# Kernel tuning notes

Measured on AMD Instinct MI355X. Metric: run time of the kernel, lower is better.

Reference implementation:

```python
import jax, jax.numpy as jnp
import numpy as np

B, D, F = 16384, 512, 28
GIN = D + D + F + 1  # 1053
EPS = 1e-5


def setup_inputs() -> dict:
    key = jax.random.key(0)
    ks = jax.random.split(key, 16)
    s = 0.02
    return {
        "team_embedding": jax.random.normal(ks[0], (B, D), jnp.float32),
        "opponent_embedding": jax.random.normal(ks[1], (B, D), jnp.float32),
        "game_features": jax.random.normal(ks[2], (B, F), jnp.float32),
        "won": jnp.round(jax.random.uniform(ks[3], (B, 1), jnp.float32)),
        # input_projection Linear(GIN -> D)
        "W_proj": jax.random.normal(ks[4], (D, GIN), jnp.float32) * s,
        "b_proj": jnp.zeros((D,), jnp.float32),
        # GRUCell params (PyTorch layout: [3D, *] with r,z,n blocks)
        "W_ih": jax.random.normal(ks[5], (3 * D, D), jnp.float32) * s,
        "b_ih": jnp.zeros((3 * D,), jnp.float32),
        "W_hh": jax.random.normal(ks[6], (3 * D, D), jnp.float32) * s,
        "b_hh": jnp.zeros((3 * D,), jnp.float32),
        # LayerNorm
        "gamma": jnp.ones((D,), jnp.float32),
        "beta": jnp.zeros((D,), jnp.float32),
        # game_importance MLP: D -> 128 -> 1
        "W_imp1": jax.random.normal(ks[7], (128, D), jnp.float32) * s,
        "b_imp1": jnp.zeros((128,), jnp.float32),
        "W_imp2": jax.random.normal(ks[8], (1, 128), jnp.float32) * s,
        "b_imp2": jnp.zeros((1,), jnp.float32),
    }


def reference(team_embedding, opponent_embedding, game_features, won,
              W_proj, b_proj, W_ih, b_ih, W_hh, b_hh,
              gamma, beta, W_imp1, b_imp1, W_imp2, b_imp2):
    # combined: [B, 2D+F+1]
    x = jnp.concatenate([team_embedding, opponent_embedding, game_features, won], axis=-1)
    # input_projection: Linear -> ReLU (Dropout is identity in eval)
    projected = jax.nn.relu(x @ W_proj.T + b_proj)  # [B, D]
    # game_importance: Linear -> ReLU -> Linear -> Sigmoid
    importance = jax.nn.sigmoid(jax.nn.relu(projected @ W_imp1.T + b_imp1) @ W_imp2.T + b_imp2)  # [B, 1]
    # GRUCell (PyTorch math)
    gi = projected @ W_ih.T + b_ih          # [B, 3D]
    gh = team_embedding @ W_hh.T + b_hh     # [B, 3D]
    i_r, i_z, i_n = jnp.split(gi, 3, axis=-1)
    h_r, h_z, h_n = jnp.split(gh, 3, axis=-1)
    r = jax.nn.sigmoid(i_r + h_r)
    z = jax.nn.sigmoid(i_z + h_z)
    n = jnp.tanh(i_n + r * h_n)
    new_embedding = (1.0 - z) * n + z * team_embedding
    # gated blend
    updated = team_embedding + importance * (new_embedding - team_embedding)
    # LayerNorm
    mu = jnp.mean(updated, axis=-1, keepdims=True)
    var = jnp.mean(jnp.square(updated - mu), axis=-1, keepdims=True)
    updated = gamma * (updated - mu) * jax.lax.rsqrt(var + EPS) + beta
    game_context = jax.lax.stop_gradient(projected)  # .detach().clone()
    return (updated, game_context)
```

## Files before the change

### kernel.cpp

```cpp
#include <hip/hip_runtime.h>
#include <hip/hip_bf16.h>


#define NB 16384
#define GINP 1088

typedef __bf16 bf16x8 __attribute__((ext_vector_type(8)));
typedef float f32x4 __attribute__((ext_vector_type(4)));
typedef unsigned short ushort8 __attribute__((ext_vector_type(8)));

__device__ __forceinline__ void gload_lds16(const void* g, void* l) {
  __builtin_amdgcn_global_load_lds(
      (const __attribute__((address_space(1))) void*)g,
      (__attribute__((address_space(3))) void*)l, 16, 0, 0);
}
__device__ __forceinline__ bf16x8 ds_read128(const unsigned short* l) {
  f32x4 r;
  asm volatile("ds_read_b128 %0, %1"
               : "=v"(r)
               : "v"((const __attribute__((address_space(3))) void*)l));
  bf16x8 out;
  __builtin_memcpy(&out, &r, 16);
  return out;
}
__device__ __forceinline__ float sigmoidf_(float x) { return 1.0f / (1.0f + expf(-x)); }
__device__ __forceinline__ float bf2f(unsigned short u) {
  unsigned int x = ((unsigned int)u) << 16;
  float f; __builtin_memcpy(&f, &x, 4); return f;
}

__global__ __launch_bounds__(256) void prep_x2(
    const float* __restrict__ team, const float* __restrict__ opp,
    const float* __restrict__ gf, const float* __restrict__ won,
    __hip_bfloat16* __restrict__ X) {
  long idx = (long)blockIdx.x * 256 + threadIdx.x;
  if (idx >= (long)NB * 136) return;
  const int r = (int)(idx / 136);
  const int c8 = (int)(idx % 136) * 8;
  float v[8];
  if (c8 < 512) {
    float4 a = *(const float4*)&team[(size_t)r * 512 + c8];
    float4 b = *(const float4*)&team[(size_t)r * 512 + c8 + 4];
    v[0]=a.x; v[1]=a.y; v[2]=a.z; v[3]=a.w; v[4]=b.x; v[5]=b.y; v[6]=b.z; v[7]=b.w;
  } else if (c8 < 1024) {
    float4 a = *(const float4*)&opp[(size_t)r * 512 + (c8 - 512)];
    float4 b = *(const float4*)&opp[(size_t)r * 512 + (c8 - 512) + 4];
    v[0]=a.x; v[1]=a.y; v[2]=a.z; v[3]=a.w; v[4]=b.x; v[5]=b.y; v[6]=b.z; v[7]=b.w;
  } else if (c8 < 1048) {
    const int g0 = c8 - 1024;
#pragma unroll
    for (int e = 0; e < 8; ++e) v[e] = gf[(size_t)r * 28 + g0 + e];
  } else if (c8 == 1048) {
    v[0] = gf[(size_t)r * 28 + 24]; v[1] = gf[(size_t)r * 28 + 25];
    v[2] = gf[(size_t)r * 28 + 26]; v[3] = gf[(size_t)r * 28 + 27];
    v[4] = won[r]; v[5] = 0.f; v[6] = 0.f; v[7] = 0.f;
  } else {
#pragma unroll
    for (int e = 0; e < 8; ++e) v[e] = 0.f;
  }
  __hip_bfloat16 h[8];
#pragma unroll
  for (int e = 0; e < 8; ++e) h[e] = __float2bfloat16(v[e]);
  *(uint4*)&X[(size_t)r * GINP + c8] = *(const uint4*)h;
}

__global__ __launch_bounds__(256) void prep_w2(
    const float* __restrict__ Wproj, const float* __restrict__ Wih,
    const float* __restrict__ Whh, const float* __restrict__ Wimp1,
    const float* __restrict__ bih, const float* __restrict__ bhh,
    __hip_bfloat16* __restrict__ Wpb, __hip_bfloat16* __restrict__ Wrz,
    __hip_bfloat16* __restrict__ Wn, __hip_bfloat16* __restrict__ Wimp1b,
    float* __restrict__ bcat) {
  long idx = (long)blockIdx.x * 256 + threadIdx.x;
  if (idx < 512L * 1088) {
    int r = (int)(idx / 1088), c = (int)(idx % 1088);
    Wpb[idx] = __float2bfloat16(c < 1053 ? Wproj[(size_t)r * 1053 + c] : 0.f);
    return;
  }
  idx -= 512L * 1088;
  if (idx < 1024L * 1024) {
    int q = (int)(idx >> 10), c = (int)(idx & 1023);
    float v = (c < 512) ? Wih[(size_t)q * 512 + c] : Whh[(size_t)q * 512 + (c - 512)];
    Wrz[idx] = __float2bfloat16(v);
    return;
  }
  idx -= 1024L * 1024;
  if (idx < 1024L * 512) {
    int q = (int)(idx / 512), c = (int)(idx % 512);
    float v = (q < 512) ? Wih[(size_t)(1024 + q) * 512 + c]
                        : Whh[(size_t)(1024 + q - 512) * 512 + c];
    Wn[idx] = __float2bfloat16(v);
    return;
  }
  idx -= 1024L * 512;
  if (idx < 128L * 512) { Wimp1b[idx] = __float2bfloat16(Wimp1[idx]); return; }
  idx -= 128L * 512;
  if (idx < 2048) {
    int j = (int)idx;
    float v;
    if (j < 1024) v = bih[j] + bhh[j];
    else if (j < 1536) v = bih[j];
    else v = bhh[j - 512];
    bcat[j] = v;
  }
}

template <int MODE>
__global__ __launch_bounds__(512, 1) void gemm_dp3(
    const __hip_bfloat16* __restrict__ A0, int lda0,
    const __hip_bfloat16* __restrict__ A1, int lda1,
    const __hip_bfloat16* __restrict__ W0, const __hip_bfloat16* __restrict__ W1,
    const float* __restrict__ bias,
    float* __restrict__ Cf, __hip_bfloat16* __restrict__ Cb,
    int tilesN, int NTP) {
  __shared__ __align__(16) unsigned short ldsA[3 * 256 * 64];
  __shared__ __align__(16) unsigned short ldsB[3 * 128 * 64];

  const int tid = threadIdx.x;
  const int wid = tid >> 6, lane = tid & 63;
  const int wr = wid >> 1, wc = wid & 1;
  const int fl = lane & 15, kh = lane >> 4;

  int bid = blockIdx.x;
  { const int cpx = gridDim.x >> 3; bid = (bid & 7) * cpx + (bid >> 3); }
  const int tm = bid / tilesN, tn = bid % tilesN;
  const int m0 = tm * 256;

  const __hip_bfloat16* Wp; int ldw, NT;
  if (MODE == 0) { Wp = W0 + (size_t)tn * 128 * GINP; ldw = GINP; NT = NTP; }
  else {
    if (tn < 8) { Wp = W0 + (size_t)tn * 128 * 1024; ldw = 1024; NT = 16; }
    else        { Wp = W1 + (size_t)(tn - 8) * 128 * 512; ldw = 512; NT = 8; }
  }
  const float* bp = bias + tn * 128;

  const int prow_b = tid >> 3;
  const int gp = tid & 7;

  auto stageAB = [&](int s, int buf) {
    const int kW = s * 64;
    const __hip_bfloat16* Ap; int lda; int kA;
    if (MODE == 0) { Ap = A0; lda = lda0; kA = s * 64; }
    else if (tn < 8) {
      if (s < 8) { Ap = A0; lda = lda0; kA = s * 64; }
      else       { Ap = A1; lda = lda1; kA = (s - 8) * 64; }
    } else if (tn < 12) { Ap = A0; lda = lda0; kA = s * 64; }
    else                { Ap = A1; lda = lda1; kA = s * 64; }
    unsigned short* la = &ldsA[buf * (256 * 64)];
    unsigned short* lb = &ldsB[buf * (128 * 64)];
#pragma unroll
    for (int i = 0; i < 4; ++i) {
      const int prow = i * 64 + prow_b;
      const int gl = gp ^ (prow & 7);
      gload_lds16(Ap + (size_t)(m0 + prow) * lda + kA + gl * 8,
                  la + i * 4096 + wid * 512);
    }
#pragma unroll
    for (int i = 0; i < 2; ++i) {
      const int prow = i * 64 + prow_b;
      const int gl = gp ^ (prow & 7);
      gload_lds16(Wp + (size_t)prow * ldw + kW + gl * 8,
                  lb + i * 4096 + wid * 512);
    }
  };

  f32x4 acc[4][4];
#pragma unroll
  for (int m = 0; m < 4; ++m)
#pragma unroll
    for (int n = 0; n < 4; ++n) acc[m][n] = (f32x4){0.f, 0.f, 0.f, 0.f};

  stageAB(0, 0);
  stageAB(1, 1);

  for (int t = 0; t < NT; ++t) {
    const int cur = t % 3;
    if (t + 1 < NT) {
      asm volatile("s_waitcnt vmcnt(6)" ::: "memory");
    } else {
      asm volatile("s_waitcnt vmcnt(0)" ::: "memory");
    }
    __builtin_amdgcn_s_barrier();
    if (t + 2 < NT) stageAB(t + 2, (t + 2) % 3);

    const unsigned short* At = &ldsA[cur * (256 * 64)];
    const unsigned short* Bt = &ldsB[cur * (128 * 64)];
    bf16x8 af[2][4], bfr[2][4];
#pragma unroll
    for (int kk = 0; kk < 2; ++kk) {
#pragma unroll
      for (int m = 0; m < 4; ++m) {
        const int r = wr * 64 + m * 16 + fl;
        const int g = (kk * 4 + kh) ^ (r & 7);
        af[kk][m] = ds_read128(&At[r * 64 + g * 8]);
      }
#pragma unroll
      for (int n = 0; n < 4; ++n) {
        const int r = wc * 64 + n * 16 + fl;
        const int g = (kk * 4 + kh) ^ (r & 7);
        bfr[kk][n] = ds_read128(&Bt[r * 64 + g * 8]);
      }
    }
    asm volatile("s_waitcnt lgkmcnt(0)" ::: "memory");
    __builtin_amdgcn_sched_barrier(0);
    __builtin_amdgcn_s_setprio(1);
#pragma unroll
    for (int kk = 0; kk < 2; ++kk)
#pragma unroll
      for (int m = 0; m < 4; ++m)
#pragma unroll
        for (int n = 0; n < 4; ++n)
          acc[m][n] = __builtin_amdgcn_mfma_f32_16x16x32_bf16(af[kk][m], bfr[kk][n], acc[m][n], 0, 0, 0);
    __builtin_amdgcn_s_setprio(0);
  }

#pragma unroll
  for (int m = 0; m < 4; ++m)
#pragma unroll
    for (int n = 0; n < 4; ++n)
#pragma unroll
      for (int j = 0; j < 4; ++j) {
        const int lrow = wr * 64 + m * 16 + kh * 4 + j;
        const int lcol = wc * 64 + n * 16 + fl;
        const size_t grow = (size_t)(m0 + lrow);
        float v = acc[m][n][j] + bp[lcol];
        if (MODE == 0) {
          v = fmaxf(v, 0.f);
          Cf[grow * 512 + tn * 128 + lcol] = v;
          Cb[grow * 512 + tn * 128 + lcol] = __float2bfloat16(v);
        } else {
          Cb[grow * 2048 + tn * 128 + lcol] = __float2bfloat16(v);
        }
      }
}

__global__ __launch_bounds__(256, 2) void gemm_imp2(
    const __hip_bfloat16* __restrict__ A, const __hip_bfloat16* __restrict__ W,
    const float* __restrict__ bias, const float* __restrict__ w2,
    const float* __restrict__ b2, float* __restrict__ imp) {
  __shared__ __align__(16) unsigned short ldsA[64 * 64];
  __shared__ __align__(16) unsigned short ldsB[128 * 64];
  __shared__ float sdot[64];
  const int tid = threadIdx.x;
  const int w = tid >> 6, lane = tid & 63;
  const int wr = w >> 1, wc = w & 1;
  const int fl = lane & 15, kh = lane >> 4;
  const int srow = lane >> 3, scol = (lane & 7) * 8;
  const int m0 = blockIdx.x * 64;

  if (tid < 64) sdot[tid] = 0.f;

  f32x4 acc[2][4];
#pragma unroll
  for (int m = 0; m < 2; ++m)
#pragma unroll
    for (int n = 0; n < 4; ++n) acc[m][n] = (f32x4){0.f, 0.f, 0.f, 0.f};

  for (int kt = 0; kt < 8; ++kt) {
    const int k0 = kt * 64;
#pragma unroll
    for (int c = 0; c < 2; ++c) {
      const int rgrp = c * 4 + w;
      const int row = rgrp * 8 + srow;
      gload_lds16(A + (size_t)(m0 + row) * 512 + k0 + scol, (char*)ldsA + rgrp * 1024);
    }
#pragma unroll
    for (int c = 0; c < 4; ++c) {
      const int rgrp = c * 4 + w;
      const int row = rgrp * 8 + srow;
      gload_lds16(W + (size_t)row * 512 + k0 + scol, (char*)ldsB + rgrp * 1024);
    }
    __syncthreads();
#pragma unroll
    for (int kk = 0; kk < 2; ++kk) {
      bf16x8 af[2], bfr[4];
#pragma unroll
      for (int m = 0; m < 2; ++m)
        af[m] = *(const bf16x8*)&ldsA[(wr * 32 + m * 16 + fl) * 64 + kk * 32 + kh * 8];
#pragma unroll
      for (int n = 0; n < 4; ++n)
        bfr[n] = *(const bf16x8*)&ldsB[(wc * 64 + n * 16 + fl) * 64 + kk * 32 + kh * 8];
#pragma unroll
      for (int m = 0; m < 2; ++m)
#pragma unroll
        for (int n = 0; n < 4; ++n)
          acc[m][n] = __builtin_amdgcn_mfma_f32_16x16x32_bf16(af[m], bfr[n], acc[m][n], 0, 0, 0);
    }
    __syncthreads();
  }
#pragma unroll
  for (int m = 0; m < 2; ++m)
#pragma unroll
    for (int j = 0; j < 4; ++j) {
      float p = 0.f;
#pragma unroll
      for (int n = 0; n < 4; ++n) {
        const int lcol = wc * 64 + n * 16 + fl;
        const float v = fmaxf(acc[m][n][j] + bias[lcol], 0.f);
        p += v * w2[lcol];
      }
      atomicAdd(&sdot[wr * 32 + m * 16 + kh * 4 + j], p);
    }
  __syncthreads();
  if (tid < 64) imp[m0 + tid] = sigmoidf_(sdot[tid] + b2[0]);
}

__global__ __launch_bounds__(256) void fuse_final2(
    const float* __restrict__ team, const __hip_bfloat16* __restrict__ gg,
    const float* __restrict__ imp, const float* __restrict__ gamma,
    const float* __restrict__ beta, float* __restrict__ out) {
  const int row = blockIdx.x * 4 + (threadIdx.x >> 6);
  const int lane = threadIdx.x & 63;
  const size_t gb = (size_t)row * 2048 + lane * 8;
  ushort8 sr = *(const ushort8*)&gg[gb];
  ushort8 szv = *(const ushort8*)&gg[gb + 512];
  ushort8 inn = *(const ushort8*)&gg[gb + 1024];
  ushort8 hnn = *(const ushort8*)&gg[gb + 1536];
  float4 t0 = *(const float4*)&team[(size_t)row * 512 + lane * 8];
  float4 t1 = *(const float4*)&team[(size_t)row * 512 + lane * 8 + 4];
  const float im = imp[row];
  float tv[8] = {t0.x, t0.y, t0.z, t0.w, t1.x, t1.y, t1.z, t1.w};
  float u[8];
  float s = 0.f, ss = 0.f;
#pragma unroll
  for (int e = 0; e < 8; ++e) {
    const float rg = sigmoidf_(bf2f(sr[e]));
    const float zg = sigmoidf_(bf2f(szv[e]));
    const float ng = tanhf(bf2f(inn[e]) + rg * bf2f(hnn[e]));
    const float ne = (1.f - zg) * ng + zg * tv[e];
    const float uu = tv[e] + im * (ne - tv[e]);
    u[e] = uu; s += uu; ss += uu * uu;
  }
#pragma unroll
  for (int off = 32; off; off >>= 1) {
    s += __shfl_down(s, off);
    ss += __shfl_down(ss, off);
  }
  s = __shfl(s, 0); ss = __shfl(ss, 0);
  const float mu = s * (1.f / 512.f);
  const float inv = rsqrtf(ss * (1.f / 512.f) - mu * mu + 1e-5f);
  float4 g0 = *(const float4*)&gamma[lane * 8], g1 = *(const float4*)&gamma[lane * 8 + 4];
  float4 b0 = *(const float4*)&beta[lane * 8], b1 = *(const float4*)&beta[lane * 8 + 4];
  float gv[8] = {g0.x, g0.y, g0.z, g0.w, g1.x, g1.y, g1.z, g1.w};
  float bv[8] = {b0.x, b0.y, b0.z, b0.w, b1.x, b1.y, b1.z, b1.w};
  float4 o0, o1;
  o0.x = gv[0] * (u[0] - mu) * inv + bv[0];
  o0.y = gv[1] * (u[1] - mu) * inv + bv[1];
  o0.z = gv[2] * (u[2] - mu) * inv + bv[2];
  o0.w = gv[3] * (u[3] - mu) * inv + bv[3];
  o1.x = gv[4] * (u[4] - mu) * inv + bv[4];
  o1.y = gv[5] * (u[5] - mu) * inv + bv[5];
  o1.z = gv[6] * (u[6] - mu) * inv + bv[6];
  o1.w = gv[7] * (u[7] - mu) * inv + bv[7];
  *(float4*)&out[(size_t)row * 512 + lane * 8] = o0;
  *(float4*)&out[(size_t)row * 512 + lane * 8 + 4] = o1;
}

extern "C" void kernel_launch(void* const* d_in, const int* in_sizes, int n_in,
                              void* d_out, int out_size, void* d_ws, size_t ws_size,
                              hipStream_t stream) {
  const float* team   = (const float*)d_in[0];
  const float* opp    = (const float*)d_in[1];
  const float* gf     = (const float*)d_in[2];
  const float* won    = (const float*)d_in[3];
  const float* W_proj = (const float*)d_in[4];
  const float* b_proj = (const float*)d_in[5];
  const float* W_ih   = (const float*)d_in[6];
  const float* b_ih   = (const float*)d_in[7];
  const float* W_hh   = (const float*)d_in[8];
  const float* b_hh   = (const float*)d_in[9];
  const float* gamma  = (const float*)d_in[10];
  const float* beta   = (const float*)d_in[11];
  const float* W_imp1 = (const float*)d_in[12];
  const float* b_imp1 = (const float*)d_in[13];
  const float* W_imp2 = (const float*)d_in[14];
  const float* b_imp2 = (const float*)d_in[15];

  char* ws = (char*)d_ws;
  size_t o = 0;
  __hip_bfloat16* Xbf    = (__hip_bfloat16*)(ws + o); o += (size_t)NB * GINP * 2;
  __hip_bfloat16* Wpb    = (__hip_bfloat16*)(ws + o); o += (size_t)512 * GINP * 2;
  __hip_bfloat16* Wrz    = (__hip_bfloat16*)(ws + o); o += (size_t)1024 * 1024 * 2;
  __hip_bfloat16* Wn     = (__hip_bfloat16*)(ws + o); o += (size_t)1024 * 512 * 2;
  __hip_bfloat16* Wimp1b = (__hip_bfloat16*)(ws + o); o += (size_t)128 * 512 * 2;
  float*          bcat   = (float*)(ws + o);          o += (size_t)2048 * 4;
  __hip_bfloat16* Pbf    = (__hip_bfloat16*)(ws + o); o += (size_t)NB * 512 * 2;
  float*          imp    = (float*)(ws + o);          o += (size_t)NB * 4;
  __hip_bfloat16* gg     = (__hip_bfloat16*)(ws + o); o += (size_t)NB * 2048 * 2;

  float* out_updated = (float*)d_out;
  float* out_ctx     = (float*)d_out + (size_t)NB * 512;

  prep_x2<<<(NB * 136 + 255) / 256, 256, 0, stream>>>(team, opp, gf, won, Xbf);
  {
    const long total = 512L * 1088 + 1024L * 1024 + 1024L * 512 + 128L * 512 + 2048;
    prep_w2<<<(int)((total + 255) / 256), 256, 0, stream>>>(
        W_proj, W_ih, W_hh, W_imp1, b_ih, b_hh, Wpb, Wrz, Wn, Wimp1b, bcat);
  }
  gemm_dp3<0><<<256, 512, 0, stream>>>(Xbf, GINP, nullptr, 0, Wpb, nullptr, b_proj,
                                       out_ctx, Pbf, 4, 17);
  gemm_imp2<<<NB / 64, 256, 0, stream>>>(Pbf, Wimp1b, b_imp1, W_imp2, b_imp2, imp);
  gemm_dp3<2><<<1024, 512, 0, stream>>>(Pbf, 512, Xbf, GINP, Wrz, Wn, bcat,
                                        nullptr, gg, 16, 0);
  fuse_final2<<<NB / 4, 256, 0, stream>>>(team, gg, imp, gamma, beta, out_updated);
}
```

Before: 157.5 us.

## Replace GRU gate GEMM with 256x256-tile kernel using phased double-buffer schedule

Adds a dedicated GRU gate GEMM kernel with 256x256 output tiles (8 waves, each owning 128x64) instead of 256x128. It double-buffers LDS and splits each K-step into four MFMA phases, interleaving LDS reads and global prefetches between them. The goal is more arithmetic per byte loaded and better overlap of loads with MFMA. The larger tile raises register pressure (128 accumulator floats per lane) and halves the grid to 512 blocks, which may leave CUs unevenly loaded.

```diff
diff --git a/kernel.cpp b/kernel.cpp
--- a/kernel.cpp
+++ b/kernel.cpp
@@ -105,6 +105,158 @@
   }
 }
 
+__global__ __launch_bounds__(512, 1) void gemm_g8(
+    const __hip_bfloat16* __restrict__ Pm, const __hip_bfloat16* __restrict__ Xb,
+    const __hip_bfloat16* __restrict__ Wrz, const __hip_bfloat16* __restrict__ Wn,
+    const float* __restrict__ bcat, __hip_bfloat16* __restrict__ gg) {
+  __shared__ __align__(16) unsigned short ldsA[2 * 256 * 64];
+  __shared__ __align__(16) unsigned short ldsB[2 * 256 * 64];
+
+  const int tid = threadIdx.x;
+  const int wid = tid >> 6, lane = tid & 63;
+  const int wr = wid >> 2, wc = wid & 3;
+  const int fl = lane & 15, kh = lane >> 4;
+  const int srow = tid >> 3;
+  const int sgp = tid & 7;
+
+  const int tn = blockIdx.x & 7, tm = blockIdx.x >> 3;
+  const int m0 = tm * 256;
+
+  const __hip_bfloat16* Wp;
+  int ldw, NT;
+  if (tn < 4) { Wp = Wrz + (size_t)tn * 256 * 1024; ldw = 1024; NT = 16; }
+  else        { Wp = Wn + (size_t)(tn - 4) * 256 * 512; ldw = 512; NT = 8; }
+  const float* bp = bcat + tn * 256;
+
+  auto stageA64 = [&](int s, int r0) {
+    const __hip_bfloat16* Ap; int lda; int k0;
+    if (tn < 4) {
+      if (s < 8) { Ap = Pm; lda = 512; k0 = s * 64; }
+      else       { Ap = Xb; lda = GINP; k0 = (s - 8) * 64; }
+    } else if (tn < 6) { Ap = Pm; lda = 512; k0 = s * 64; }
+    else               { Ap = Xb; lda = GINP; k0 = s * 64; }
+    const int row = r0 + srow;
+    const int gl = sgp ^ (row & 7);
+    gload_lds16(Ap + (size_t)(m0 + row) * lda + k0 + gl * 8,
+                &ldsA[(s & 1) * 16384 + (r0 + (wid << 3)) * 64]);
+  };
+  auto stageB64 = [&](int s, int r0) {
+    const int row = r0 + srow;
+    const int gl = sgp ^ (row & 7);
+    gload_lds16(Wp + (size_t)row * ldw + s * 64 + gl * 8,
+                &ldsB[(s & 1) * 16384 + (r0 + (wid << 3)) * 64]);
+  };
+  auto readA = [&](int sl, int m, int kk) -> bf16x8 {
+    const int row = wr * 128 + m * 16 + fl;
+    const int g = (kk * 4 + kh) ^ (row & 7);
+    return ds_read128(&ldsA[sl + row * 64 + g * 8]);
+  };
+  auto readB = [&](int sl, int n, int kk) -> bf16x8 {
+    const int row = wc * 64 + n * 16 + fl;
+    const int g = (kk * 4 + kh) ^ (row & 7);
+    return ds_read128(&ldsB[sl + row * 64 + g * 8]);
+  };
+
+  f32x4 acc[8][4];
+#pragma unroll
+  for (int m = 0; m < 8; ++m)
+#pragma unroll
+    for (int n = 0; n < 4; ++n) acc[m][n] = (f32x4){0.f, 0.f, 0.f, 0.f};
+
+  stageA64(0, 0); stageA64(0, 64); stageA64(0, 128); stageA64(0, 192);
+  stageB64(0, 0); stageB64(0, 64); stageB64(0, 128); stageB64(0, 192);
+  stageA64(1, 0); stageA64(1, 64); stageA64(1, 128); stageA64(1, 192);
+  stageB64(1, 0); stageB64(1, 64); stageB64(1, 128); stageB64(1, 192);
+  asm volatile("s_waitcnt vmcnt(8)" ::: "memory");
+  __builtin_amdgcn_s_barrier();
+
+  for (int t = 0; t < NT; ++t) {
+    const int sl = (t & 1) * 16384;
+    const bool pf = (t + 2 < NT);
+    bf16x8 fa0[4][2], fa1[4][2], fb0[2][2], fb1[2][2];
+
+#pragma unroll
+    for (int m = 0; m < 4; ++m) { fa0[m][0] = readA(sl, m, 0); fa0[m][1] = readA(sl, m, 1); }
+#pragma unroll
+    for (int n = 0; n < 2; ++n) { fb0[n][0] = readB(sl, n, 0); fb0[n][1] = readB(sl, n, 1); }
+    __builtin_amdgcn_s_barrier();
+    asm volatile("s_waitcnt lgkmcnt(0)" ::: "memory");
+    __builtin_amdgcn_sched_barrier(0);
+    __builtin_amdgcn_s_setprio(1);
+#pragma unroll
+    for (int kk = 0; kk < 2; ++kk)
+#pragma unroll
+      for (int m = 0; m < 4; ++m)
+#pragma unroll
+        for (int n = 0; n < 2; ++n)
+          acc[m][n] = __builtin_amdgcn_mfma_f32_16x16x32_bf16(fa0[m][kk], fb0[n][kk], acc[m][n], 0, 0, 0);
+    __builtin_amdgcn_s_setprio(0);
+    __builtin_amdgcn_s_barrier();
+
+#pragma unroll
+    for (int m = 0; m < 4; ++m) { fa1[m][0] = readA(sl, m + 4, 0); fa1[m][1] = readA(sl, m + 4, 1); }
+    if (pf) { stageA64(t + 2, 0); stageA64(t + 2, 128); }
+    __builtin_amdgcn_s_barrier();
+    asm volatile("s_waitcnt lgkmcnt(0)" ::: "memory");
+    __builtin_amdgcn_sched_barrier(0);
+    __builtin_amdgcn_s_setprio(1);
+#pragma unroll
+    for (int kk = 0; kk < 2; ++kk)
+#pragma unroll
+      for (int m = 0; m < 4; ++m)
+#pragma unroll
+        for (int n = 0; n < 2; ++n)
+          acc[m + 4][n] = __builtin_amdgcn_mfma_f32_16x16x32_bf16(fa1[m][kk], fb0[n][kk], acc[m + 4][n], 0, 0, 0);
+    __builtin_amdgcn_s_setprio(0);
+    __builtin_amdgcn_s_barrier();
+
+#pragma unroll
+    for (int n = 0; n < 2; ++n) { fb1[n][0] = readB(sl, n + 2, 0); fb1[n][1] = readB(sl, n + 2, 1); }
+    if (pf) { stageA64(t + 2, 64); stageA64(t + 2, 192); }
+    __builtin_amdgcn_s_barrier();
+    asm volatile("s_waitcnt lgkmcnt(0)" ::: "memory");
+    __builtin_amdgcn_sched_barrier(0);
+    __builtin_amdgcn_s_setprio(1);
+#pragma unroll
+    for (int kk = 0; kk < 2; ++kk)
+#pragma unroll
+      for (int m = 0; m < 4; ++m)
+#pragma unroll
+        for (int n = 0; n < 2; ++n)
+          acc[m + 4][n + 2] = __builtin_amdgcn_mfma_f32_16x16x32_bf16(fa1[m][kk], fb1[n][kk], acc[m + 4][n + 2], 0, 0, 0);
+    __builtin_amdgcn_s_setprio(0);
+    __builtin_amdgcn_s_barrier();
+
+    if (pf) { stageB64(t + 2, 0); stageB64(t + 2, 64); stageB64(t + 2, 128); stageB64(t + 2, 192); }
+    __builtin_amdgcn_sched_barrier(0);
+    __builtin_amdgcn_s_barrier();
+    __builtin_amdgcn_s_setprio(1);
+#pragma unroll
+    for (int kk = 0; kk < 2; ++kk)
+#pragma unroll
+      for (int m = 0; m < 4; ++m)
+#pragma unroll
+        for (int n = 0; n < 2; ++n)
+          acc[m][n + 2] = __builtin_amdgcn_mfma_f32_16x16x32_bf16(fa0[m][kk], fb1[n][kk], acc[m][n + 2], 0, 0, 0);
+    __builtin_amdgcn_s_setprio(0);
+    if (pf) { asm volatile("s_waitcnt vmcnt(8)" ::: "memory"); }
+    else    { asm volatile("s_waitcnt vmcnt(0)" ::: "memory"); }
+    __builtin_amdgcn_s_barrier();
+  }
+
+#pragma unroll
+  for (int m = 0; m < 8; ++m)
+#pragma unroll
+    for (int n = 0; n < 4; ++n)
+#pragma unroll
+      for (int j = 0; j < 4; ++j) {
+        const int lrow = wr * 128 + m * 16 + kh * 4 + j;
+        const int lcol = wc * 64 + n * 16 + fl;
+        gg[(size_t)(m0 + lrow) * 2048 + tn * 256 + lcol] =
+            __float2bfloat16(acc[m][n][j] + bp[lcol]);
+      }
+}
+
 template <int MODE>
 __global__ __launch_bounds__(512, 1) void gemm_dp3(
     const __hip_bfloat16* __restrict__ A0, int lda0,
@@ -127,11 +279,7 @@
   const int m0 = tm * 256;
 
   const __hip_bfloat16* Wp; int ldw, NT;
-  if (MODE == 0) { Wp = W0 + (size_t)tn * 128 * GINP; ldw = GINP; NT = NTP; }
-  else {
-    if (tn < 8) { Wp = W0 + (size_t)tn * 128 * 1024; ldw = 1024; NT = 16; }
-    else        { Wp = W1 + (size_t)(tn - 8) * 128 * 512; ldw = 512; NT = 8; }
-  }
+  Wp = W0 + (size_t)tn * 128 * GINP; ldw = GINP; NT = NTP;
   const float* bp = bias + tn * 128;
 
   const int prow_b = tid >> 3;
@@ -139,13 +287,7 @@
 
   auto stageAB = [&](int s, int buf) {
     const int kW = s * 64;
-    const __hip_bfloat16* Ap; int lda; int kA;
-    if (MODE == 0) { Ap = A0; lda = lda0; kA = s * 64; }
-    else if (tn < 8) {
-      if (s < 8) { Ap = A0; lda = lda0; kA = s * 64; }
-      else       { Ap = A1; lda = lda1; kA = (s - 8) * 64; }
-    } else if (tn < 12) { Ap = A0; lda = lda0; kA = s * 64; }
-    else                { Ap = A1; lda = lda1; kA = s * 64; }
+    const __hip_bfloat16* Ap = A0; int lda = lda0; int kA = s * 64;
     unsigned short* la = &ldsA[buf * (256 * 64)];
     unsigned short* lb = &ldsB[buf * (128 * 64)];
 #pragma unroll
@@ -175,11 +317,8 @@
 
   for (int t = 0; t < NT; ++t) {
     const int cur = t % 3;
-    if (t + 1 < NT) {
-      asm volatile("s_waitcnt vmcnt(6)" ::: "memory");
-    } else {
-      asm volatile("s_waitcnt vmcnt(0)" ::: "memory");
-    }
+    if (t + 1 < NT) { asm volatile("s_waitcnt vmcnt(6)" ::: "memory"); }
+    else            { asm volatile("s_waitcnt vmcnt(0)" ::: "memory"); }
     __builtin_amdgcn_s_barrier();
     if (t + 2 < NT) stageAB(t + 2, (t + 2) % 3);
 
@@ -224,13 +363,9 @@
         const int lcol = wc * 64 + n * 16 + fl;
         const size_t grow = (size_t)(m0 + lrow);
         float v = acc[m][n][j] + bp[lcol];
-        if (MODE == 0) {
-          v = fmaxf(v, 0.f);
-          Cf[grow * 512 + tn * 128 + lcol] = v;
-          Cb[grow * 512 + tn * 128 + lcol] = __float2bfloat16(v);
-        } else {
-          Cb[grow * 2048 + tn * 128 + lcol] = __float2bfloat16(v);
-        }
+        v = fmaxf(v, 0.f);
+        Cf[grow * 512 + tn * 128 + lcol] = v;
+        Cb[grow * 512 + tn * 128 + lcol] = __float2bfloat16(v);
       }
 }
 
@@ -400,7 +535,6 @@
   gemm_dp3<0><<<256, 512, 0, stream>>>(Xbf, GINP, nullptr, 0, Wpb, nullptr, b_proj,
                                        out_ctx, Pbf, 4, 17);
   gemm_imp2<<<NB / 64, 256, 0, stream>>>(Pbf, Wimp1b, b_imp1, W_imp2, b_imp2, imp);
-  gemm_dp3<2><<<1024, 512, 0, stream>>>(Pbf, 512, Xbf, GINP, Wrz, Wn, bcat,
-                                        nullptr, gg, 16, 0);
+  gemm_g8<<<512, 512, 0, stream>>>(Pbf, Xbf, Wrz, Wn, bcat, gg);
   fuse_final2<<<NB / 4, 256, 0, stream>>>(team, gg, imp, gamma, beta, out_updated);
 }
```

Result: slower. 169.8 us (+7.8%).

## Shrink GEMM tiles to 128x128 with double buffering and merge prep kernels

Applied to the files above, without the earlier changes.

The GEMM kernel moves from 256x128 tiles, 512 threads and a triple-buffered LDS pipeline to 128x128 tiles, 256 threads and double buffering, with launch bounds allowing two blocks per CU. Grid sizes double to keep coverage. The two prep kernels become one launch to save a launch. Each k-step now waits for all outstanding loads (vmcnt(0)), so load-compute overlap is shallower, and A-tile reuse drops. This trade is made for occupancy and more blocks.

```diff
diff --git a/kernel.cpp b/kernel.cpp
--- a/kernel.cpp
+++ b/kernel.cpp
@@ -29,49 +29,50 @@
   float f; __builtin_memcpy(&f, &x, 4); return f;
 }
 
-__global__ __launch_bounds__(256) void prep_x2(
+#define PREP_X_BLOCKS ((NB * 136 + 255) / 256)
+__global__ __launch_bounds__(256) void prep_all(
     const float* __restrict__ team, const float* __restrict__ opp,
     const float* __restrict__ gf, const float* __restrict__ won,
-    __hip_bfloat16* __restrict__ X) {
-  long idx = (long)blockIdx.x * 256 + threadIdx.x;
-  if (idx >= (long)NB * 136) return;
-  const int r = (int)(idx / 136);
-  const int c8 = (int)(idx % 136) * 8;
-  float v[8];
-  if (c8 < 512) {
-    float4 a = *(const float4*)&team[(size_t)r * 512 + c8];
-    float4 b = *(const float4*)&team[(size_t)r * 512 + c8 + 4];
-    v[0]=a.x; v[1]=a.y; v[2]=a.z; v[3]=a.w; v[4]=b.x; v[5]=b.y; v[6]=b.z; v[7]=b.w;
-  } else if (c8 < 1024) {
-    float4 a = *(const float4*)&opp[(size_t)r * 512 + (c8 - 512)];
-    float4 b = *(const float4*)&opp[(size_t)r * 512 + (c8 - 512) + 4];
-    v[0]=a.x; v[1]=a.y; v[2]=a.z; v[3]=a.w; v[4]=b.x; v[5]=b.y; v[6]=b.z; v[7]=b.w;
-  } else if (c8 < 1048) {
-    const int g0 = c8 - 1024;
-#pragma unroll
-    for (int e = 0; e < 8; ++e) v[e] = gf[(size_t)r * 28 + g0 + e];
-  } else if (c8 == 1048) {
-    v[0] = gf[(size_t)r * 28 + 24]; v[1] = gf[(size_t)r * 28 + 25];
-    v[2] = gf[(size_t)r * 28 + 26]; v[3] = gf[(size_t)r * 28 + 27];
-    v[4] = won[r]; v[5] = 0.f; v[6] = 0.f; v[7] = 0.f;
-  } else {
-#pragma unroll
-    for (int e = 0; e < 8; ++e) v[e] = 0.f;
-  }
-  __hip_bfloat16 h[8];
-#pragma unroll
-  for (int e = 0; e < 8; ++e) h[e] = __float2bfloat16(v[e]);
-  *(uint4*)&X[(size_t)r * GINP + c8] = *(const uint4*)h;
-}
-
-__global__ __launch_bounds__(256) void prep_w2(
     const float* __restrict__ Wproj, const float* __restrict__ Wih,
     const float* __restrict__ Whh, const float* __restrict__ Wimp1,
     const float* __restrict__ bih, const float* __restrict__ bhh,
+    __hip_bfloat16* __restrict__ X,
     __hip_bfloat16* __restrict__ Wpb, __hip_bfloat16* __restrict__ Wrz,
     __hip_bfloat16* __restrict__ Wn, __hip_bfloat16* __restrict__ Wimp1b,
     float* __restrict__ bcat) {
-  long idx = (long)blockIdx.x * 256 + threadIdx.x;
+  if (blockIdx.x < PREP_X_BLOCKS) {
+    long idx = (long)blockIdx.x * 256 + threadIdx.x;
+    if (idx >= (long)NB * 136) return;
+    const int r = (int)(idx / 136);
+    const int c8 = (int)(idx % 136) * 8;
+    float v[8];
+    if (c8 < 512) {
+      float4 a = *(const float4*)&team[(size_t)r * 512 + c8];
+      float4 b = *(const float4*)&team[(size_t)r * 512 + c8 + 4];
+      v[0]=a.x; v[1]=a.y; v[2]=a.z; v[3]=a.w; v[4]=b.x; v[5]=b.y; v[6]=b.z; v[7]=b.w;
+    } else if (c8 < 1024) {
+      float4 a = *(const float4*)&opp[(size_t)r * 512 + (c8 - 512)];
+      float4 b = *(const float4*)&opp[(size_t)r * 512 + (c8 - 512) + 4];
+      v[0]=a.x; v[1]=a.y; v[2]=a.z; v[3]=a.w; v[4]=b.x; v[5]=b.y; v[6]=b.z; v[7]=b.w;
+    } else if (c8 < 1048) {
+      const int g0 = c8 - 1024;
+#pragma unroll
+      for (int e = 0; e < 8; ++e) v[e] = gf[(size_t)r * 28 + g0 + e];
+    } else if (c8 == 1048) {
+      v[0] = gf[(size_t)r * 28 + 24]; v[1] = gf[(size_t)r * 28 + 25];
+      v[2] = gf[(size_t)r * 28 + 26]; v[3] = gf[(size_t)r * 28 + 27];
+      v[4] = won[r]; v[5] = 0.f; v[6] = 0.f; v[7] = 0.f;
+    } else {
+#pragma unroll
+      for (int e = 0; e < 8; ++e) v[e] = 0.f;
+    }
+    __hip_bfloat16 h[8];
+#pragma unroll
+    for (int e = 0; e < 8; ++e) h[e] = __float2bfloat16(v[e]);
+    *(uint4*)&X[(size_t)r * GINP + c8] = *(const uint4*)h;
+    return;
+  }
+  long idx = (long)(blockIdx.x - PREP_X_BLOCKS) * 256 + threadIdx.x;
   if (idx < 512L * 1088) {
     int r = (int)(idx / 1088), c = (int)(idx % 1088);
     Wpb[idx] = __float2bfloat16(c < 1053 ? Wproj[(size_t)r * 1053 + c] : 0.f);
@@ -106,25 +107,27 @@
 }
 
 template <int MODE>
-__global__ __launch_bounds__(512, 1) void gemm_dp3(
+__global__ __launch_bounds__(256, 2) void gemm_r2(
     const __hip_bfloat16* __restrict__ A0, int lda0,
     const __hip_bfloat16* __restrict__ A1, int lda1,
     const __hip_bfloat16* __restrict__ W0, const __hip_bfloat16* __restrict__ W1,
     const float* __restrict__ bias,
     float* __restrict__ Cf, __hip_bfloat16* __restrict__ Cb,
     int tilesN, int NTP) {
-  __shared__ __align__(16) unsigned short ldsA[3 * 256 * 64];
-  __shared__ __align__(16) unsigned short ldsB[3 * 128 * 64];
+  __shared__ __align__(16) unsigned short ldsA[2 * 128 * 64];
+  __shared__ __align__(16) unsigned short ldsB[2 * 128 * 64];
 
   const int tid = threadIdx.x;
   const int wid = tid >> 6, lane = tid & 63;
   const int wr = wid >> 1, wc = wid & 1;
   const int fl = lane & 15, kh = lane >> 4;
+  const int prow_b = tid >> 3;
+  const int gp = tid & 7;
 
   int bid = blockIdx.x;
   { const int cpx = gridDim.x >> 3; bid = (bid & 7) * cpx + (bid >> 3); }
   const int tm = bid / tilesN, tn = bid % tilesN;
-  const int m0 = tm * 256;
+  const int m0 = tm * 128;
 
   const __hip_bfloat16* Wp; int ldw, NT;
   if (MODE == 0) { Wp = W0 + (size_t)tn * 128 * GINP; ldw = GINP; NT = NTP; }
@@ -134,10 +137,7 @@
   }
   const float* bp = bias + tn * 128;
 
-  const int prow_b = tid >> 3;
-  const int gp = tid & 7;
-
-  auto stageAB = [&](int s, int buf) {
+  auto stage = [&](int s) {
     const int kW = s * 64;
     const __hip_bfloat16* Ap; int lda; int kA;
     if (MODE == 0) { Ap = A0; lda = lda0; kA = s * 64; }
@@ -146,21 +146,16 @@
       else       { Ap = A1; lda = lda1; kA = (s - 8) * 64; }
     } else if (tn < 12) { Ap = A0; lda = lda0; kA = s * 64; }
     else                { Ap = A1; lda = lda1; kA = s * 64; }
-    unsigned short* la = &ldsA[buf * (256 * 64)];
-    unsigned short* lb = &ldsB[buf * (128 * 64)];
+    unsigned short* la = &ldsA[(s & 1) * 8192];
+    unsigned short* lb = &ldsB[(s & 1) * 8192];
 #pragma unroll
     for (int i = 0; i < 4; ++i) {
-      const int prow = i * 64 + prow_b;
-      const int gl = gp ^ (prow & 7);
-      gload_lds16(Ap + (size_t)(m0 + prow) * lda + kA + gl * 8,
-                  la + i * 4096 + wid * 512);
-    }
-#pragma unroll
-    for (int i = 0; i < 2; ++i) {
-      const int prow = i * 64 + prow_b;
-      const int gl = gp ^ (prow & 7);
-      gload_lds16(Wp + (size_t)prow * ldw + kW + gl * 8,
-                  lb + i * 4096 + wid * 512);
+      const int row = i * 32 + prow_b;
+      const int gl = gp ^ (row & 7);
+      gload_lds16(Ap + (size_t)(m0 + row) * lda + kA + gl * 8,
+                  la + (i * 32 + wid * 8) * 64);
+      gload_lds16(Wp + (size_t)row * ldw + kW + gl * 8,
+                  lb + (i * 32 + wid * 8) * 64);
     }
   };
 
@@ -170,21 +165,14 @@
 #pragma unroll
     for (int n = 0; n < 4; ++n) acc[m][n] = (f32x4){0.f, 0.f, 0.f, 0.f};
 
-  stageAB(0, 0);
-  stageAB(1, 1);
+  stage(0);
 
   for (int t = 0; t < NT; ++t) {
-    const int cur = t % 3;
-    if (t + 1 < NT) {
-      asm volatile("s_waitcnt vmcnt(6)" ::: "memory");
-    } else {
-      asm volatile("s_waitcnt vmcnt(0)" ::: "memory");
-    }
+    const int sl = (t & 1) * 8192;
+    asm volatile("s_waitcnt vmcnt(0)" ::: "memory");
     __builtin_amdgcn_s_barrier();
-    if (t + 2 < NT) stageAB(t + 2, (t + 2) % 3);
-
-    const unsigned short* At = &ldsA[cur * (256 * 64)];
-    const unsigned short* Bt = &ldsB[cur * (128 * 64)];
+    if (t + 1 < NT) stage(t + 1);
+
     bf16x8 af[2][4], bfr[2][4];
 #pragma unroll
     for (int kk = 0; kk < 2; ++kk) {
@@ -192,13 +180,13 @@
       for (int m = 0; m < 4; ++m) {
         const int r = wr * 64 + m * 16 + fl;
         const int g = (kk * 4 + kh) ^ (r & 7);
-        af[kk][m] = ds_read128(&At[r * 64 + g * 8]);
+        af[kk][m] = ds_read128(&ldsA[sl + r * 64 + g * 8]);
       }
 #pragma unroll
       for (int n = 0; n < 4; ++n) {
         const int r = wc * 64 + n * 16 + fl;
         const int g = (kk * 4 + kh) ^ (r & 7);
-        bfr[kk][n] = ds_read128(&Bt[r * 64 + g * 8]);
+        bfr[kk][n] = ds_read128(&ldsB[sl + r * 64 + g * 8]);
       }
     }
     asm volatile("s_waitcnt lgkmcnt(0)" ::: "memory");
@@ -391,16 +379,17 @@
   float* out_updated = (float*)d_out;
   float* out_ctx     = (float*)d_out + (size_t)NB * 512;
 
-  prep_x2<<<(NB * 136 + 255) / 256, 256, 0, stream>>>(team, opp, gf, won, Xbf);
   {
-    const long total = 512L * 1088 + 1024L * 1024 + 1024L * 512 + 128L * 512 + 2048;
-    prep_w2<<<(int)((total + 255) / 256), 256, 0, stream>>>(
-        W_proj, W_ih, W_hh, W_imp1, b_ih, b_hh, Wpb, Wrz, Wn, Wimp1b, bcat);
-  }
-  gemm_dp3<0><<<256, 512, 0, stream>>>(Xbf, GINP, nullptr, 0, Wpb, nullptr, b_proj,
-                                       out_ctx, Pbf, 4, 17);
+    const long wtotal = 512L * 1088 + 1024L * 1024 + 1024L * 512 + 128L * 512 + 2048;
+    const int wblocks = (int)((wtotal + 255) / 256);
+    prep_all<<<PREP_X_BLOCKS + wblocks, 256, 0, stream>>>(
+        team, opp, gf, won, W_proj, W_ih, W_hh, W_imp1, b_ih, b_hh,
+        Xbf, Wpb, Wrz, Wn, Wimp1b, bcat);
+  }
+  gemm_r2<0><<<512, 256, 0, stream>>>(Xbf, GINP, nullptr, 0, Wpb, nullptr, b_proj,
+                                      out_ctx, Pbf, 4, 17);
   gemm_imp2<<<NB / 64, 256, 0, stream>>>(Pbf, Wimp1b, b_imp1, W_imp2, b_imp2, imp);
-  gemm_dp3<2><<<1024, 512, 0, stream>>>(Pbf, 512, Xbf, GINP, Wrz, Wn, bcat,
-                                        nullptr, gg, 16, 0);
+  gemm_r2<2><<<2048, 256, 0, stream>>>(Pbf, 512, Xbf, GINP, Wrz, Wn, bcat,
+                                       nullptr, gg, 16, 0);
   fuse_final2<<<NB / 4, 256, 0, stream>>>(team, gg, imp, gamma, beta, out_updated);
 }
```

After: 150.7 us. 1.05x faster.
